# Kernel tuning notes

Hardware: AMD Instinct MI355X
Metric: run time of the kernel (lower is better)

The kernel has to match this reference:

```python
import jax, jax.numpy as jnp
import numpy as np

B, H, W, C = 8, 64, 64, 256
NH, WS, SS = 8, 8, 4
HD = C // NH          # head dim 32
N = WS * WS           # 64 tokens per window
NW = (H // WS) * (W // WS)  # 64 windows
MLP = 4 * C


def _rel_index():
    ch = np.arange(WS)
    coords = np.stack(np.meshgrid(ch, ch, indexing='ij')).reshape(2, -1)  # [2, N]
    rel = (coords[:, :, None] - coords[:, None, :]).transpose(1, 2, 0)   # [N, N, 2]
    rel[:, :, 0] += WS - 1
    rel[:, :, 1] += WS - 1
    rel[:, :, 0] *= 2 * WS - 1
    return jnp.asarray(rel.sum(-1))  # [N, N] indices into table

REL_IDX = _rel_index()


def _attn_mask():
    # standard Swin shifted-window mask: [nW, N, N] with 0 / -100
    img = np.zeros((H, W))
    slices = (slice(0, -WS), slice(-WS, -SS), slice(-SS, None))
    cnt = 0
    for hs in slices:
        for ws_ in slices:
            img[hs, ws_] = cnt
            cnt += 1
    m = img.reshape(H // WS, WS, W // WS, WS).transpose(0, 2, 1, 3).reshape(-1, N)
    diff = m[:, None, :] - m[:, :, None]
    return jnp.asarray(np.where(diff != 0, -100.0, 0.0).astype(np.float32))

MASK = _attn_mask()


def setup_inputs() -> dict:
    key = jax.random.key(0)
    ks = jax.random.split(key, 8)
    s = 0.02
    return {
        'hidden_states': jax.random.normal(ks[0], (B, H * W, C), jnp.float32),
        'ln1_g': jnp.ones((C,), jnp.float32),
        'ln1_b': jnp.zeros((C,), jnp.float32),
        'wq': jax.random.normal(ks[1], (C, C), jnp.float32) * s,
        'bq': jnp.zeros((C,), jnp.float32),
        'wk': jax.random.normal(ks[2], (C, C), jnp.float32) * s,
        'bk': jnp.zeros((C,), jnp.float32),
        'wv': jax.random.normal(ks[3], (C, C), jnp.float32) * s,
        'bv': jnp.zeros((C,), jnp.float32),
        'rel_table': jax.random.normal(ks[4], ((2 * WS - 1) ** 2, NH), jnp.float32) * s,
        'wo': jax.random.normal(ks[5], (C, C), jnp.float32) * s,
        'bo': jnp.zeros((C,), jnp.float32),
        'ln2_g': jnp.ones((C,), jnp.float32),
        'ln2_b': jnp.zeros((C,), jnp.float32),
        'w1': jax.random.normal(ks[6], (MLP, C), jnp.float32) * s,
        'b1': jnp.zeros((MLP,), jnp.float32),
        'w2': jax.random.normal(ks[7], (C, MLP), jnp.float32) * s,
        'b2': jnp.zeros((C,), jnp.float32),
    }


def _ln(x, g, b):
    mu = x.mean(-1, keepdims=True)
    var = x.var(-1, keepdims=True)
    return (x - mu) * jax.lax.rsqrt(var + 1e-5) * g + b


def reference(hidden_states, ln1_g, ln1_b, wq, bq, wk, bk, wv, bv, rel_table,
              wo, bo, ln2_g, ln2_b, w1, b1, w2, b2):
    shortcut = hidden_states
    x = _ln(hidden_states, ln1_g, ln1_b).reshape(B, H, W, C)
    # cyclic shift
    x = jnp.roll(x, (-SS, -SS), axis=(1, 2))
    # window partition -> [B*nW, N, C]
    xw = x.reshape(B, H // WS, WS, W // WS, WS, C).transpose(0, 1, 3, 2, 4, 5).reshape(-1, N, C)
    q = (xw @ wq.T + bq).reshape(-1, N, NH, HD).transpose(0, 2, 1, 3)
    k = (xw @ wk.T + bk).reshape(-1, N, NH, HD).transpose(0, 2, 1, 3)
    v = (xw @ wv.T + bv).reshape(-1, N, NH, HD).transpose(0, 2, 1, 3)
    scores = jnp.einsum('bhnd,bhmd->bhnm', q, k) / np.float32(np.sqrt(HD))
    bias = rel_table[REL_IDX]                 # [N, N, NH] gathered bias
    scores = scores + bias.transpose(2, 0, 1)[None]
    scores = scores.reshape(B, NW, NH, N, N) + MASK[None, :, None]
    probs = jax.nn.softmax(scores, axis=-1).reshape(-1, NH, N, N)
    ctx = jnp.einsum('bhnm,bhmd->bnhd', probs, v).reshape(-1, N, C)
    attn_out = ctx @ wo.T + bo                # SelfOutput dense
    # window reverse + reverse shift
    x = attn_out.reshape(B, H // WS, W // WS, WS, WS, C).transpose(0, 1, 3, 2, 4, 5).reshape(B, H, W, C)
    x = jnp.roll(x, (SS, SS), axis=(1, 2)).reshape(B, H * W, C)
    hidden = shortcut + x
    y = _ln(hidden, ln2_g, ln2_b)
    y = jax.nn.gelu(y @ w1.T + b1, approximate=False) @ w2.T + b2
    return hidden + y
```

## Files before the change

kernel.cpp:

```cpp
#include <hip/hip_runtime.h>
#include <hip/hip_bf16.h>
#include <math.h>

__device__ __forceinline__ unsigned short f2bf(float f) {
    union { float f; unsigned u; } c; c.f = f;
    unsigned r = c.u + 0x7fffu + ((c.u >> 16) & 1u);
    return (unsigned short)(r >> 16);
}
__device__ __forceinline__ float bfu(unsigned short u) {
    union { unsigned x; float f; } c; c.x = ((unsigned)u) << 16; return c.f;
}
__device__ __forceinline__ float gelu_t(float x) {
    float z = x * (1.59576912f + 0.07135481f * x * x);
    return x / (1.0f + __expf(-z));
}

typedef __bf16 bf16x8_t __attribute__((ext_vector_type(8)));
typedef float  f32x4_t  __attribute__((ext_vector_type(4)));

#define AS1 __attribute__((address_space(1)))
#define AS3 __attribute__((address_space(3)))
__device__ __forceinline__ void g2lds16(const void* g, void* l) {
    __builtin_amdgcn_global_load_lds((const AS1 unsigned int*)g, (AS3 unsigned int*)l, 16, 0, 0);
}

__global__ void cvt_all(const float* __restrict__ wq, const float* __restrict__ wk,
                        const float* __restrict__ wv, const float* __restrict__ wo,
                        const float* __restrict__ w1, const float* __restrict__ w2,
                        unsigned short* __restrict__ wqkv_b, unsigned short* __restrict__ wo_b,
                        unsigned short* __restrict__ w1_b, unsigned short* __restrict__ w2_b) {
    int i = blockIdx.x * 256 + threadIdx.x;
    const float* src; unsigned short* dst; int base;
    if (i < 16384)       { src = wq; dst = wqkv_b;          base = 0; }
    else if (i < 32768)  { src = wk; dst = wqkv_b + 65536;  base = 16384; }
    else if (i < 49152)  { src = wv; dst = wqkv_b + 131072; base = 32768; }
    else if (i < 65536)  { src = wo; dst = wo_b;            base = 49152; }
    else if (i < 131072) { src = w1; dst = w1_b;            base = 65536; }
    else                 { src = w2; dst = w2_b;            base = 131072; }
    int j = (i - base) * 4;
    float4 v = *(const float4*)(src + j);
    ushort4 o = { f2bf(v.x), f2bf(v.y), f2bf(v.z), f2bf(v.w) };
    *(ushort4*)(dst + j) = o;
}

template<int GATHER, int BF16IN>
__global__ void ln_kernel(const void* __restrict__ xv, const float* __restrict__ g,
                          const float* __restrict__ b, unsigned short* __restrict__ out) {
    int row  = blockIdx.x * 4 + (threadIdx.x >> 6);
    int lane = threadIdx.x & 63;
    int src;
    if (GATHER) {
        int bb = row >> 12;
        int rem = row & 4095;
        int winid = rem >> 6, tok = rem & 63;
        int wi = winid >> 3, wj = winid & 7;
        int ii = tok >> 3,  jj = tok & 7;
        int hh = (wi * 8 + ii + 4) & 63;
        int ww = (wj * 8 + jj + 4) & 63;
        src = (bb << 12) + hh * 64 + ww;
    } else {
        src = row;
    }
    float4 v;
    if (BF16IN) {
        ushort4 u = *(const ushort4*)((const unsigned short*)xv + (size_t)src * 256 + lane * 4);
        v.x = bfu(u.x); v.y = bfu(u.y); v.z = bfu(u.z); v.w = bfu(u.w);
    } else {
        v = *(const float4*)((const float*)xv + (size_t)src * 256 + lane * 4);
    }
    float s  = v.x + v.y + v.z + v.w;
    float s2 = v.x*v.x + v.y*v.y + v.z*v.z + v.w*v.w;
    #pragma unroll
    for (int off = 32; off > 0; off >>= 1) {
        s  += __shfl_xor(s,  off, 64);
        s2 += __shfl_xor(s2, off, 64);
    }
    float mean = s * (1.0f / 256.0f);
    float var  = s2 * (1.0f / 256.0f) - mean * mean;
    float rstd = rsqrtf(var + 1e-5f);
    int c0 = lane * 4;
    float4 gg  = *(const float4*)(g + c0);
    float4 bb4 = *(const float4*)(b + c0);
    ushort4 o;
    o.x = f2bf((v.x - mean) * rstd * gg.x + bb4.x);
    o.y = f2bf((v.y - mean) * rstd * gg.y + bb4.y);
    o.z = f2bf((v.z - mean) * rstd * gg.z + bb4.z);
    o.w = f2bf((v.w - mean) * rstd * gg.w + bb4.w);
    *(ushort4*)(out + (size_t)row * 256 + c0) = o;
}

template<int MODE, int K>
__global__ __launch_bounds__(256, 4) void gemm_tile(
        const unsigned short* __restrict__ A,
        const unsigned short* __restrict__ Bw,
        const float* __restrict__ bias,
        int M, int N,
        unsigned short* __restrict__ obf,
        float* __restrict__ of32,
        const void* __restrict__ addp) {
    __shared__ unsigned short As[128 * 64];
    __shared__ unsigned short Bs[128 * 64];
    const int t = threadIdx.x;
    const int lane = t & 63, wave = t >> 6;
    const int m0 = blockIdx.x * 128, n0 = blockIdx.y * 128;
    const int wm = (wave >> 1) * 64, wn = (wave & 1) * 64;
    const int lr = lane & 15, kg = lane >> 4;

    f32x4_t acc[4][4];
    #pragma unroll
    for (int i = 0; i < 4; ++i)
        #pragma unroll
        for (int j = 0; j < 4; ++j) { acc[i][j][0]=0.f; acc[i][j][1]=0.f; acc[i][j][2]=0.f; acc[i][j][3]=0.f; }

    const int srow = t >> 3;
    const int sck  = (t & 7) * 8;
    const unsigned short* ga = A  + (size_t)(m0 + srow) * K + sck;
    const unsigned short* gb = Bw + (size_t)(n0 + srow) * K + sck;
    unsigned short* la = &As[t * 8];
    unsigned short* lb = &Bs[t * 8];

    #pragma unroll
    for (int k0 = 0; k0 < K; k0 += 64) {
        __syncthreads();
        #pragma unroll
        for (int i = 0; i < 4; ++i) {
            g2lds16(ga + (size_t)(i * 32) * K + k0, la + i * 2048);
            g2lds16(gb + (size_t)(i * 32) * K + k0, lb + i * 2048);
        }
        __syncthreads();
        #pragma unroll
        for (int ks = 0; ks < 64; ks += 32) {
            bf16x8_t af[4], bfr[4];
            #pragma unroll
            for (int i = 0; i < 4; ++i)
                af[i] = *(const bf16x8_t*)&As[(wm + i * 16 + lr) * 64 + ks + kg * 8];
            #pragma unroll
            for (int j = 0; j < 4; ++j)
                bfr[j] = *(const bf16x8_t*)&Bs[(wn + j * 16 + lr) * 64 + ks + kg * 8];
            #pragma unroll
            for (int i = 0; i < 4; ++i)
                #pragma unroll
                for (int j = 0; j < 4; ++j)
                    acc[i][j] = __builtin_amdgcn_mfma_f32_16x16x32_bf16(af[i], bfr[j], acc[i][j], 0, 0, 0);
        }
    }

    #pragma unroll
    for (int i = 0; i < 4; ++i) {
        #pragma unroll
        for (int j = 0; j < 4; ++j) {
            int col = n0 + wn + j * 16 + lr;
            float bv = bias[col];
            #pragma unroll
            for (int e = 0; e < 4; ++e) {
                int row = m0 + wm + i * 16 + kg * 4 + e;
                float v = acc[i][j][e] + bv;
                if (MODE == 0) {
                    obf[(size_t)row * N + col] = f2bf(v);
                } else if (MODE == 1) {
                    obf[(size_t)row * N + col] = f2bf(gelu_t(v));
                } else if (MODE == 2) {
                    int bb = row >> 12;
                    int rem = row & 4095;
                    int winid = rem >> 6, tok = rem & 63;
                    int wi = winid >> 3, wj = winid & 7;
                    int ii = tok >> 3,  jj = tok & 7;
                    int hh = (wi * 8 + ii + 4) & 63;
                    int ww = (wj * 8 + jj + 4) & 63;
                    size_t dst = ((size_t)(bb << 12) + hh * 64 + ww) * 256 + col;
                    obf[dst] = f2bf(((const float*)addp)[dst] + v);
                } else {
                    size_t dst = (size_t)row * N + col;
                    of32[dst] = bfu(((const unsigned short*)addp)[dst]) + v;
                }
            }
        }
    }
}

#define PR 72
#define VR 72
__global__ void __launch_bounds__(256) attn_mfma(
        const unsigned short* __restrict__ qkv,
        const float* __restrict__ relt,
        unsigned short* __restrict__ ctx) {
    __shared__ float rs[1800];
    __shared__ unsigned short Pl[4][64 * PR];
    __shared__ unsigned short Vt[4][32 * VR];

    int t = threadIdx.x;
    int lane = t & 63, wave = t >> 6;
    for (int i = t; i < 1800; i += 256) rs[i] = relt[i];
    __syncthreads();

    int wh = blockIdx.x * 4 + wave;
    int wg = wh >> 3, h = wh & 7;
    int win = wg & 63;
    int ln = lane & 15, quad = lane >> 4;

    unsigned short* P = &Pl[wave][0];
    unsigned short* V = &Vt[wave][0];
    const unsigned short* base = qkv + (size_t)wg * 64 * 768 + h * 32;

    union BF8 { bf16x8_t v; unsigned short s[8]; };
    {
        const bf16x8_t* vp = (const bf16x8_t*)(base + (size_t)lane * 768 + 512);
        BF8 vv[4];
        #pragma unroll
        for (int c = 0; c < 4; ++c) vv[c].v = vp[c];
        #pragma unroll
        for (int c = 0; c < 4; ++c)
            #pragma unroll
            for (int e = 0; e < 8; ++e)
                V[(c * 8 + e) * VR + lane] = vv[c].s[e];
    }

    bf16x8_t qa[4], kb[4];
    #pragma unroll
    for (int i = 0; i < 4; ++i)
        qa[i] = *(const bf16x8_t*)(base + (size_t)(i * 16 + ln) * 768 + quad * 8);
    #pragma unroll
    for (int j = 0; j < 4; ++j)
        kb[j] = *(const bf16x8_t*)(base + (size_t)(j * 16 + ln) * 768 + 256 + quad * 8);

    f32x4_t acc[4][4];
    #pragma unroll
    for (int i = 0; i < 4; ++i)
        #pragma unroll
        for (int j = 0; j < 4; ++j) { acc[i][j][0]=0.f; acc[i][j][1]=0.f; acc[i][j][2]=0.f; acc[i][j][3]=0.f; }
    #pragma unroll
    for (int i = 0; i < 4; ++i)
        #pragma unroll
        for (int j = 0; j < 4; ++j)
            acc[i][j] = __builtin_amdgcn_mfma_f32_16x16x32_bf16(qa[i], kb[j], acc[i][j], 0, 0, 0);

    const float scale = 0.17677669529663687f;
    int wi = win >> 3, wj = win & 7;
    int mjv = ln & 7;
    int regm[4], mi[4];
    #pragma unroll
    for (int j = 0; j < 4; ++j) {
        mi[j] = j * 2 + (ln >> 3);
        int hm = wi * 8 + mi[j], wm = wj * 8 + mjv;
        regm[j] = (hm < 56 ? 0 : (hm < 60 ? 1 : 2)) * 3 + (wm < 56 ? 0 : (wm < 60 ? 1 : 2));
    }
    float inv[4][4];
    #pragma unroll
    for (int i = 0; i < 4; ++i) {
        #pragma unroll
        for (int e = 0; e < 4; ++e) {
            int q = i * 16 + quad * 4 + e;
            int ti = q >> 3, tj = q & 7;
            int hn = wi * 8 + ti, wn = wj * 8 + tj;
            int regn = (hn < 56 ? 0 : (hn < 60 ? 1 : 2)) * 3 + (wn < 56 ? 0 : (wn < 60 ? 1 : 2));
            float sum = 0.f;
            #pragma unroll
            for (int j = 0; j < 4; ++j) {
                float bv = rs[((ti - mi[j] + 7) * 15 + (tj - mjv + 7)) * 8 + h];
                float s = acc[i][j][e] * scale + bv + (regm[j] != regn ? -100.f : 0.f);
                float p = __expf(s);
                sum += p;
                P[q * PR + j * 16 + ln] = f2bf(p);
            }
            #pragma unroll
            for (int off = 1; off < 16; off <<= 1) sum += __shfl_xor(sum, off, 64);
            inv[i][e] = 1.0f / sum;
        }
    }
    __syncthreads();

    bf16x8_t vb[2][2];
    #pragma unroll
    for (int jd = 0; jd < 2; ++jd)
        #pragma unroll
        for (int kc = 0; kc < 2; ++kc)
            vb[jd][kc] = *(const bf16x8_t*)&V[(jd * 16 + ln) * VR + kc * 32 + quad * 8];
    f32x4_t occ[4][2];
    #pragma unroll
    for (int i = 0; i < 4; ++i)
        #pragma unroll
        for (int jd = 0; jd < 2; ++jd) { occ[i][jd][0]=0.f; occ[i][jd][1]=0.f; occ[i][jd][2]=0.f; occ[i][jd][3]=0.f; }
    #pragma unroll
    for (int i = 0; i < 4; ++i) {
        #pragma unroll
        for (int kc = 0; kc < 2; ++kc) {
            bf16x8_t pf = *(const bf16x8_t*)&P[(i * 16 + ln) * PR + kc * 32 + quad * 8];
            occ[i][0] = __builtin_amdgcn_mfma_f32_16x16x32_bf16(pf, vb[0][kc], occ[i][0], 0, 0, 0);
            occ[i][1] = __builtin_amdgcn_mfma_f32_16x16x32_bf16(pf, vb[1][kc], occ[i][1], 0, 0, 0);
        }
    }

    unsigned short* cbase = ctx + (size_t)wg * 64 * 256 + h * 32;
    #pragma unroll
    for (int i = 0; i < 4; ++i)
        #pragma unroll
        for (int e = 0; e < 4; ++e) {
            int q = i * 16 + quad * 4 + e;
            #pragma unroll
            for (int jd = 0; jd < 2; ++jd)
                cbase[(size_t)q * 256 + jd * 16 + ln] = f2bf(occ[i][jd][e] * inv[i][e]);
        }
}

extern "C" void kernel_launch(void* const* d_in, const int* in_sizes, int n_in,
                              void* d_out, int out_size, void* d_ws, size_t ws_size,
                              hipStream_t stream) {
    const float* hs   = (const float*)d_in[0];
    const float* ln1g = (const float*)d_in[1];
    const float* ln1b = (const float*)d_in[2];
    const float* wq   = (const float*)d_in[3];
    const float* bq   = (const float*)d_in[4];
    const float* wk   = (const float*)d_in[5];
    const float* bk   = (const float*)d_in[6];
    const float* wv   = (const float*)d_in[7];
    const float* bv   = (const float*)d_in[8];
    const float* relt = (const float*)d_in[9];
    const float* wo   = (const float*)d_in[10];
    const float* bo   = (const float*)d_in[11];
    const float* ln2g = (const float*)d_in[12];
    const float* ln2b = (const float*)d_in[13];
    const float* w1   = (const float*)d_in[14];
    const float* b1   = (const float*)d_in[15];
    const float* w2   = (const float*)d_in[16];
    const float* b2   = (const float*)d_in[17];
    float* out = (float*)d_out;

    const size_t NTOK = 32768;
    size_t off = 0;
    auto carve = [&](size_t bytes) { void* p = (char*)d_ws + off; off += (bytes + 255) & ~(size_t)255; return p; };
    unsigned short* wqkv_b = (unsigned short*)carve(768ull * 256 * 2);
    unsigned short* wo_b   = (unsigned short*)carve(65536ull * 2);
    unsigned short* w1_b   = (unsigned short*)carve(262144ull * 2);
    unsigned short* w2_b   = (unsigned short*)carve(262144ull * 2);
    float*          bqkv   = (float*)carve(768ull * 4);
    unsigned short* hiddenb= (unsigned short*)carve(NTOK * 256 * 2);
    unsigned short* xw     = (unsigned short*)carve(NTOK * 256 * 2);
    unsigned short* qkvb   = (unsigned short*)carve(NTOK * 768 * 2);
    unsigned short* cx     = (unsigned short*)carve(NTOK * 256 * 2);
    unsigned short* h1 = qkvb;
    unsigned short* yb = xw;

    cvt_all<<<768, 256, 0, stream>>>(wq, wk, wv, wo, w1, w2, wqkv_b, wo_b, w1_b, w2_b);
    hipMemcpyAsync(bqkv,       bq, 256 * 4, hipMemcpyDeviceToDevice, stream);
    hipMemcpyAsync(bqkv + 256, bk, 256 * 4, hipMemcpyDeviceToDevice, stream);
    hipMemcpyAsync(bqkv + 512, bv, 256 * 4, hipMemcpyDeviceToDevice, stream);

    ln_kernel<1, 0><<<8192, 256, 0, stream>>>(hs, ln1g, ln1b, xw);

    gemm_tile<0, 256><<<dim3(256, 6), 256, 0, stream>>>(xw, wqkv_b, bqkv, 32768, 768, qkvb, nullptr, nullptr);

    attn_mfma<<<1024, 256, 0, stream>>>(qkvb, relt, cx);

    gemm_tile<2, 256><<<dim3(256, 2), 256, 0, stream>>>(cx, wo_b, bo, 32768, 256, hiddenb, nullptr, hs);

    ln_kernel<0, 1><<<8192, 256, 0, stream>>>(hiddenb, ln2g, ln2b, yb);

    gemm_tile<1, 256><<<dim3(256, 8), 256, 0, stream>>>(yb, w1_b, b1, 32768, 1024, h1, nullptr, nullptr);

    gemm_tile<3, 1024><<<dim3(256, 2), 256, 0, stream>>>(h1, w2_b, b2, 32768, 256, nullptr, out, hiddenb);
}
```

Measured before the change: 268.7 us.

## Pad GEMM LDS tiles to avoid bank conflicts and fold bias copies into convert kernel

Changes the GEMM shared-memory layout so rows are interleaved across waves with a padded stride of 520 elements. The MFMA fragment reads then avoid the LDS bank conflicts that the unpadded 64-element row stride caused, while the direct global-to-LDS loads stay contiguous per wave. It also removes three device-to-device hipMemcpyAsync calls by adding an extra block to the weight-conversion kernel that copies the q/k/v biases. The new addressing is intricate and must map rows correctly for the fragment loads.

```diff
diff --git a/kernel.cpp b/kernel.cpp
--- a/kernel.cpp
+++ b/kernel.cpp
@@ -27,8 +27,18 @@
 __global__ void cvt_all(const float* __restrict__ wq, const float* __restrict__ wk,
                         const float* __restrict__ wv, const float* __restrict__ wo,
                         const float* __restrict__ w1, const float* __restrict__ w2,
+                        const float* __restrict__ bq, const float* __restrict__ bk,
+                        const float* __restrict__ bv,
                         unsigned short* __restrict__ wqkv_b, unsigned short* __restrict__ wo_b,
-                        unsigned short* __restrict__ w1_b, unsigned short* __restrict__ w2_b) {
+                        unsigned short* __restrict__ w1_b, unsigned short* __restrict__ w2_b,
+                        float* __restrict__ bqkv) {
+    if (blockIdx.x == 768) {
+        int t = threadIdx.x;
+        bqkv[t]       = bq[t];
+        bqkv[256 + t] = bk[t];
+        bqkv[512 + t] = bv[t];
+        return;
+    }
     int i = blockIdx.x * 256 + threadIdx.x;
     const float* src; unsigned short* dst; int base;
     if (i < 16384)       { src = wq; dst = wqkv_b;          base = 0; }
@@ -98,8 +108,8 @@
         unsigned short* __restrict__ obf,
         float* __restrict__ of32,
         const void* __restrict__ addp) {
-    __shared__ unsigned short As[128 * 64];
-    __shared__ unsigned short Bs[128 * 64];
+    __shared__ unsigned short As[16 * 520];
+    __shared__ unsigned short Bs[16 * 520];
     const int t = threadIdx.x;
     const int lane = t & 63, wave = t >> 6;
     const int m0 = blockIdx.x * 128, n0 = blockIdx.y * 128;
@@ -112,20 +122,20 @@
         #pragma unroll
         for (int j = 0; j < 4; ++j) { acc[i][j][0]=0.f; acc[i][j][1]=0.f; acc[i][j][2]=0.f; acc[i][j][3]=0.f; }
 
-    const int srow = t >> 3;
-    const int sck  = (t & 7) * 8;
+    const int srow = wave + 16 * (lane >> 3);
+    const int sck  = (lane & 7) * 8;
     const unsigned short* ga = A  + (size_t)(m0 + srow) * K + sck;
     const unsigned short* gb = Bw + (size_t)(n0 + srow) * K + sck;
-    unsigned short* la = &As[t * 8];
-    unsigned short* lb = &Bs[t * 8];
+    unsigned short* la = &As[wave * 520 + lane * 8];
+    unsigned short* lb = &Bs[wave * 520 + lane * 8];
 
     #pragma unroll
     for (int k0 = 0; k0 < K; k0 += 64) {
         __syncthreads();
         #pragma unroll
         for (int i = 0; i < 4; ++i) {
-            g2lds16(ga + (size_t)(i * 32) * K + k0, la + i * 2048);
-            g2lds16(gb + (size_t)(i * 32) * K + k0, lb + i * 2048);
+            g2lds16(ga + (size_t)(i * 4) * K + k0, la + i * 2080);
+            g2lds16(gb + (size_t)(i * 4) * K + k0, lb + i * 2080);
         }
         __syncthreads();
         #pragma unroll
@@ -133,10 +143,10 @@
             bf16x8_t af[4], bfr[4];
             #pragma unroll
             for (int i = 0; i < 4; ++i)
-                af[i] = *(const bf16x8_t*)&As[(wm + i * 16 + lr) * 64 + ks + kg * 8];
+                af[i] = *(const bf16x8_t*)&As[lr * 520 + wm * 4 + i * 64 + ks + kg * 8];
             #pragma unroll
             for (int j = 0; j < 4; ++j)
-                bfr[j] = *(const bf16x8_t*)&Bs[(wn + j * 16 + lr) * 64 + ks + kg * 8];
+                bfr[j] = *(const bf16x8_t*)&Bs[lr * 520 + wn * 4 + j * 64 + ks + kg * 8];
             #pragma unroll
             for (int i = 0; i < 4; ++i)
                 #pragma unroll
@@ -340,10 +350,8 @@
     unsigned short* h1 = qkvb;
     unsigned short* yb = xw;
 
-    cvt_all<<<768, 256, 0, stream>>>(wq, wk, wv, wo, w1, w2, wqkv_b, wo_b, w1_b, w2_b);
-    hipMemcpyAsync(bqkv,       bq, 256 * 4, hipMemcpyDeviceToDevice, stream);
-    hipMemcpyAsync(bqkv + 256, bk, 256 * 4, hipMemcpyDeviceToDevice, stream);
-    hipMemcpyAsync(bqkv + 512, bv, 256 * 4, hipMemcpyDeviceToDevice, stream);
+    cvt_all<<<769, 256, 0, stream>>>(wq, wk, wv, wo, w1, w2, bq, bk, bv,
+                                     wqkv_b, wo_b, w1_b, w2_b, bqkv);
 
     ln_kernel<1, 0><<<8192, 256, 0, stream>>>(hs, ln1g, ln1b, xw);
 
```

Result: no change. 273.7 us (+1.9%).
